# Kernel tuning notes

Hardware: AMD Instinct MI355X
Metric: run time of the kernel (lower is better)

## Reference

```python
import jax, jax.numpy as jnp
import numpy as np

B, N, C = 4, 1024, 256
E = 65536
HID = 256  # LAYERS = [256, 256, 256]

def _linear_init(key, out_dim, in_dim):
    kw, kb = jax.random.split(key)
    s = 1.0 / np.sqrt(in_dim)
    W = jax.random.uniform(kw, (out_dim, in_dim), jnp.float32, -s, s)
    b = jax.random.uniform(kb, (out_dim,), jnp.float32, -s, s)
    return W, b

def setup_inputs() -> dict:
    key = jax.random.key(0)
    ks = jax.random.split(key, 5)
    pooled_features = jax.random.normal(ks[0], (B, N, C), jnp.float32)
    edge_index = jax.random.randint(ks[1], (2, E), 0, B * N)  # [src; dst]
    W1, b1 = _linear_init(ks[2], HID, 2 * C)
    W2, b2 = _linear_init(ks[3], HID, 2 * HID)
    W3, b3 = _linear_init(ks[4], HID, 2 * HID)
    return {"pooled_features": pooled_features, "edge_index": edge_index,
            "W1": W1, "b1": b1, "W2": W2, "b2": b2, "W3": W3, "b3": b3}

def _edge_conv(x, src, dst, num_nodes, W, b):
    # PyG EdgeConv: x_j = x[src], x_i = x[dst]; msg = relu(fc([x_j - x_i, x_i]));
    # aggr='max' scatters messages onto dst nodes.
    x_i = x[dst]                                   # [E, d]
    x_j = x[src]                                   # [E, d]
    msg = jnp.concatenate([x_j - x_i, x_i], axis=-1)  # [E, 2d]
    msg = jax.nn.relu(msg @ W.T + b)               # [E, out]
    out = jax.ops.segment_max(msg, dst, num_segments=num_nodes)
    # empty segments -> -inf; PyG fills with 0, and relu messages are >= 0
    return jnp.maximum(out, 0.0)

def reference(pooled_features, edge_index, W1, b1, W2, b2, W3, b3):
    b_, n_, c_ = pooled_features.shape
    num_nodes = b_ * n_
    x = pooled_features.reshape(num_nodes, c_)
    src, dst = edge_index[0], edge_index[1]
    feats = [x]
    for W, bb in ((W1, b1), (W2, b2), (W3, b3)):
        x = _edge_conv(x, src, dst, num_nodes, W, bb)
        feats.append(x)
    related_features = jnp.concatenate(feats, axis=-1)  # [num_nodes, 1024]
    return related_features
```

## Files before the change

### kernel.cpp

```cpp
#include <hip/hip_runtime.h>


#define NODES 4096
#define EDGES 65536
#define OSTR 1024
#define DEGCAP 64

typedef __attribute__((ext_vector_type(8))) short bf16x8;
typedef __attribute__((ext_vector_type(4))) float f32x4;

__device__ __forceinline__ unsigned short f2bf(float f) {
    unsigned int x = __float_as_uint(f);
    return (unsigned short)((x + 0x7fff + ((x >> 16) & 1)) >> 16);
}
__device__ __forceinline__ float bf2f(unsigned short u) {
    return __uint_as_float(((unsigned int)u) << 16);
}

__device__ __forceinline__ void gemm_phase(int l, const short* Alds,
                                           const short* __restrict__ Wp,
                                           const float* __restrict__ bias,
                                           unsigned short* __restrict__ UWu,
                                           float* __restrict__ UWw,
                                           int b, int t) {
    const int wv = t >> 6, lane = t & 63;
    const int lm = lane & 15, kq = lane >> 4;
    const int nhalf = wv >> 3, sub = wv & 7;
    f32x4 acc0 = (f32x4){0.f, 0.f, 0.f, 0.f};
    f32x4 acc1 = (f32x4){0.f, 0.f, 0.f, 0.f};
    const short* ap = Alds + lm * 264 + kq * 8;
    const short* bp = Wp + (size_t)l * 131072
                         + (size_t)(nhalf * 256 + sub * 32 + lm) * 256 + kq * 8;
#pragma unroll
    for (int ks = 0; ks < 8; ++ks) {
        const int ko = ks * 32;
        bf16x8 a  = *(const bf16x8*)(ap + ko);
        bf16x8 q0 = *(const bf16x8*)(bp + ko);
        bf16x8 q1 = *(const bf16x8*)(bp + 16 * 256 + ko);
        acc0 = __builtin_amdgcn_mfma_f32_16x16x32_bf16(a, q0, acc0, 0, 0, 0);
        acc1 = __builtin_amdgcn_mfma_f32_16x16x32_bf16(a, q1, acc1, 0, 0, 0);
    }
    unsigned short* UW = UWu + (size_t)(l & 1) * NODES * 256;
#pragma unroll
    for (int nt2 = 0; nt2 < 2; ++nt2) {
        int nc = sub * 32 + nt2 * 16 + lm;
        f32x4 av = nt2 ? acc1 : acc0;
        if (nhalf == 0) {
#pragma unroll
            for (int p = 0; p < 4; ++p)
                UW[(size_t)(b * 16 + kq * 4 + p) * 256 + nc] = f2bf(av[p]);
        } else {
            float bc = bias[nc];
#pragma unroll
            for (int p = 0; p < 4; ++p)
                UWw[(size_t)(b * 16 + kq * 4 + p) * 256 + nc] = av[p] + bc;
        }
    }
}

__device__ __forceinline__ void edge_phase(int l,
                                           const unsigned short* __restrict__ UWu,
                                           const float* __restrict__ UWw,
                                           const int* __restrict__ cursor,
                                           const int* __restrict__ srcS,
                                           float* __restrict__ out,
                                           short* AldsW, int b, int t) {
    const int wv = t >> 6, lane = t & 63;
    const int i = b * 16 + wv;
    int deg = cursor[i]; if (deg > DEGCAP) deg = DEGCAP;
    const int beg = i * DEGCAP, end = beg + deg;
    const unsigned short* UW = UWu + (size_t)(l & 1) * NODES * 256;
    const float NEG = -3.4e38f;
    float mx0 = NEG, mx1 = NEG, mx2 = NEG, mx3 = NEG;
    int e = beg;
    for (; e + 8 <= end; e += 8) {
        int s0 = srcS[e + 0], s1 = srcS[e + 1], s2 = srcS[e + 2], s3 = srcS[e + 3];
        int s4 = srcS[e + 4], s5 = srcS[e + 5], s6 = srcS[e + 6], s7 = srcS[e + 7];
        ushort4 v0 = *(const ushort4*)(UW + (size_t)s0 * 256 + lane * 4);
        ushort4 v1 = *(const ushort4*)(UW + (size_t)s1 * 256 + lane * 4);
        ushort4 v2 = *(const ushort4*)(UW + (size_t)s2 * 256 + lane * 4);
        ushort4 v3 = *(const ushort4*)(UW + (size_t)s3 * 256 + lane * 4);
        ushort4 v4 = *(const ushort4*)(UW + (size_t)s4 * 256 + lane * 4);
        ushort4 v5 = *(const ushort4*)(UW + (size_t)s5 * 256 + lane * 4);
        ushort4 v6 = *(const ushort4*)(UW + (size_t)s6 * 256 + lane * 4);
        ushort4 v7 = *(const ushort4*)(UW + (size_t)s7 * 256 + lane * 4);
        mx0 = fmaxf(mx0, fmaxf(fmaxf(bf2f(v0.x), bf2f(v1.x)), fmaxf(bf2f(v2.x), bf2f(v3.x))));
        mx0 = fmaxf(mx0, fmaxf(fmaxf(bf2f(v4.x), bf2f(v5.x)), fmaxf(bf2f(v6.x), bf2f(v7.x))));
        mx1 = fmaxf(mx1, fmaxf(fmaxf(bf2f(v0.y), bf2f(v1.y)), fmaxf(bf2f(v2.y), bf2f(v3.y))));
        mx1 = fmaxf(mx1, fmaxf(fmaxf(bf2f(v4.y), bf2f(v5.y)), fmaxf(bf2f(v6.y), bf2f(v7.y))));
        mx2 = fmaxf(mx2, fmaxf(fmaxf(bf2f(v0.z), bf2f(v1.z)), fmaxf(bf2f(v2.z), bf2f(v3.z))));
        mx2 = fmaxf(mx2, fmaxf(fmaxf(bf2f(v4.z), bf2f(v5.z)), fmaxf(bf2f(v6.z), bf2f(v7.z))));
        mx3 = fmaxf(mx3, fmaxf(fmaxf(bf2f(v0.w), bf2f(v1.w)), fmaxf(bf2f(v2.w), bf2f(v3.w))));
        mx3 = fmaxf(mx3, fmaxf(fmaxf(bf2f(v4.w), bf2f(v5.w)), fmaxf(bf2f(v6.w), bf2f(v7.w))));
    }
    for (; e + 4 <= end; e += 4) {
        int s0 = srcS[e + 0], s1 = srcS[e + 1], s2 = srcS[e + 2], s3 = srcS[e + 3];
        ushort4 v0 = *(const ushort4*)(UW + (size_t)s0 * 256 + lane * 4);
        ushort4 v1 = *(const ushort4*)(UW + (size_t)s1 * 256 + lane * 4);
        ushort4 v2 = *(const ushort4*)(UW + (size_t)s2 * 256 + lane * 4);
        ushort4 v3 = *(const ushort4*)(UW + (size_t)s3 * 256 + lane * 4);
        mx0 = fmaxf(mx0, fmaxf(fmaxf(bf2f(v0.x), bf2f(v1.x)), fmaxf(bf2f(v2.x), bf2f(v3.x))));
        mx1 = fmaxf(mx1, fmaxf(fmaxf(bf2f(v0.y), bf2f(v1.y)), fmaxf(bf2f(v2.y), bf2f(v3.y))));
        mx2 = fmaxf(mx2, fmaxf(fmaxf(bf2f(v0.z), bf2f(v1.z)), fmaxf(bf2f(v2.z), bf2f(v3.z))));
        mx3 = fmaxf(mx3, fmaxf(fmaxf(bf2f(v0.w), bf2f(v1.w)), fmaxf(bf2f(v2.w), bf2f(v3.w))));
    }
    for (; e < end; ++e) {
        int s = srcS[e];
        ushort4 v = *(const ushort4*)(UW + (size_t)s * 256 + lane * 4);
        mx0 = fmaxf(mx0, bf2f(v.x)); mx1 = fmaxf(mx1, bf2f(v.y));
        mx2 = fmaxf(mx2, bf2f(v.z)); mx3 = fmaxf(mx3, bf2f(v.w));
    }
    float4 w4 = *(const float4*)(UWw + (size_t)i * 256 + lane * 4);
    f32x4 r;
    r[0] = fmaxf(mx0 + w4.x, 0.0f);
    r[1] = fmaxf(mx1 + w4.y, 0.0f);
    r[2] = fmaxf(mx2 + w4.z, 0.0f);
    r[3] = fmaxf(mx3 + w4.w, 0.0f);
    *(f32x4*)(out + (size_t)i * OSTR + (l + 1) * 256 + lane * 4) = r;
    if (AldsW) {
        ushort4 rb;
        rb.x = f2bf(r[0]); rb.y = f2bf(r[1]); rb.z = f2bf(r[2]); rb.w = f2bf(r[3]);
        *(ushort4*)(AldsW + wv * 264 + lane * 4) = rb;
    }
}

__global__ __launch_bounds__(256) void k_prep(const float* __restrict__ x0,
                                              const int* __restrict__ srcIdx,
                                              const int* __restrict__ dstIdx,
                                              const float* __restrict__ W0,
                                              const float* __restrict__ W1,
                                              const float* __restrict__ W2,
                                              float* __restrict__ out,
                                              short* __restrict__ Wp,
                                              int* __restrict__ cursor,
                                              int* __restrict__ srcS) {
    int tid = blockIdx.x * 256 + threadIdx.x;
    f32x4 v = ((const f32x4*)x0)[tid];
    ((f32x4*)out)[(size_t)(tid >> 6) * 256 + (tid & 63)] = v;
    for (int q = tid; q < 393216; q += 262144) {
        int layer = q >> 17, idx = q & 131071;
        const float* W = layer == 0 ? W0 : (layer == 1 ? W1 : W2);
        int n2 = idx >> 8, c = idx & 255;
        float wv2 = (n2 < 256) ? W[n2 * 512 + c]
                               : W[(n2 - 256) * 512 + 256 + c] - W[(n2 - 256) * 512 + c];
        Wp[q] = (short)f2bf(wv2);
    }
    if (tid < EDGES) {
        int d = dstIdx[tid];
        int p = atomicAdd(&cursor[d], 1);
        if (p < DEGCAP) srcS[d * DEGCAP + p] = srcIdx[tid];
    }
}

__global__ __launch_bounds__(1024, 4) void k_g0(const float* __restrict__ x0,
                                                const short* __restrict__ Wp,
                                                const float* __restrict__ B0,
                                                unsigned short* __restrict__ UWu,
                                                float* __restrict__ UWw) {
    __shared__ __align__(16) short Alds[16 * 264];
    const int t = threadIdx.x, b = blockIdx.x;
    {
        int row = t >> 6, c4 = t & 63;
        f32x4 v = *((const f32x4*)x0 + (size_t)(b * 16 + row) * 64 + c4);
        ushort4 hb;
        hb.x = f2bf(v[0]); hb.y = f2bf(v[1]); hb.z = f2bf(v[2]); hb.w = f2bf(v[3]);
        *(ushort4*)(Alds + row * 264 + c4 * 4) = hb;
    }
    __syncthreads();
    gemm_phase(0, Alds, Wp, B0, UWu, UWw, b, t);
}

__global__ __launch_bounds__(1024, 4) void k_eg(int l,
                                                const short* __restrict__ Wp,
                                                const float* __restrict__ biasN,
                                                unsigned short* __restrict__ UWu,
                                                float* __restrict__ UWw,
                                                const int* __restrict__ cursor,
                                                const int* __restrict__ srcS,
                                                float* __restrict__ out) {
    __shared__ __align__(16) short Alds[16 * 264];
    const int t = threadIdx.x, b = blockIdx.x;
    edge_phase(l, UWu, UWw, cursor, srcS, out, Alds, b, t);
    __syncthreads();
    gemm_phase(l + 1, Alds, Wp, biasN, UWu, UWw, b, t);
}

__global__ __launch_bounds__(1024, 4) void k_e2(const unsigned short* __restrict__ UWu,
                                                const float* __restrict__ UWw,
                                                const int* __restrict__ cursor,
                                                const int* __restrict__ srcS,
                                                float* __restrict__ out) {
    const int t = threadIdx.x, b = blockIdx.x;
    edge_phase(2, UWu, UWw, cursor, srcS, out, (short*)nullptr, b, t);
}

extern "C" void kernel_launch(void* const* d_in, const int* in_sizes, int n_in,
                              void* d_out, int out_size, void* d_ws, size_t ws_size,
                              hipStream_t stream) {
    const float* x0 = (const float*)d_in[0];
    const int* ei = (const int*)d_in[1];
    const int* srcIdx = ei;
    const int* dstIdx = ei + EDGES;
    float* out = (float*)d_out;

    char* w = (char*)d_ws;
    unsigned short* UWu = (unsigned short*)w;
    float* UWw = (float*)(w + 4194304);
    short* Wp = (short*)(w + 8388608);
    int* srcS = (int*)(w + 9175040);
    int* cursor = (int*)(w + 10223616);

    (void)hipMemsetAsync((void*)cursor, 0, 16384, stream);

    const float* W0 = (const float*)d_in[2]; const float* B0 = (const float*)d_in[3];
    const float* W1 = (const float*)d_in[4]; const float* B1 = (const float*)d_in[5];
    const float* W2 = (const float*)d_in[6]; const float* B2 = (const float*)d_in[7];

    k_prep<<<1024, 256, 0, stream>>>(x0, srcIdx, dstIdx, W0, W1, W2, out, Wp, cursor, srcS);
    k_g0<<<256, 1024, 0, stream>>>(x0, Wp, B0, UWu, UWw);
    k_eg<<<256, 1024, 0, stream>>>(0, Wp, B1, UWu, UWw, cursor, srcS, out);
    k_eg<<<256, 1024, 0, stream>>>(1, Wp, B2, UWu, UWw, cursor, srcS, out);
    k_e2<<<256, 1024, 0, stream>>>(UWu, UWw, cursor, srcS, out);
}
```

Measured before the change: 132.1 us.

## Fuse prep into first GEMM kernel and preload weight fragments into registers

Merges the prep kernel (input copy, CSR build, weight packing) with the layer-0 GEMM into one launch. Layer-0 weights are read straight from fp32 W0 and converted to bf16 in registers, so only layers 1-2 are packed into Wp, which shrinks the workspace. In the edge+GEMM kernels, each wave loads its weight fragments into registers before the edge phase so that the load latency overlaps the gather. The cost is more register pressure under 1024-thread blocks, and each layer-0 block redundantly re-reads and converts W0 from fp32.

After: 150.6 us. 1.14x slower.

```diff
diff --git a/kernel.cpp b/kernel.cpp
--- a/kernel.cpp
+++ b/kernel.cpp
@@ -16,31 +16,34 @@
 __device__ __forceinline__ float bf2f(unsigned short u) {
     return __uint_as_float(((unsigned int)u) << 16);
 }
-
-__device__ __forceinline__ void gemm_phase(int l, const short* Alds,
-                                           const short* __restrict__ Wp,
-                                           const float* __restrict__ bias,
-                                           unsigned short* __restrict__ UWu,
-                                           float* __restrict__ UWw,
-                                           int b, int t) {
+__device__ __forceinline__ bf16x8 pack8(float4 a, float4 b) {
+    bf16x8 r;
+    r[0] = (short)f2bf(a.x); r[1] = (short)f2bf(a.y);
+    r[2] = (short)f2bf(a.z); r[3] = (short)f2bf(a.w);
+    r[4] = (short)f2bf(b.x); r[5] = (short)f2bf(b.y);
+    r[6] = (short)f2bf(b.z); r[7] = (short)f2bf(b.w);
+    return r;
+}
+
+__device__ __forceinline__ void gemm_regs(int par, const bf16x8 fb[2][8],
+                                          const short* Alds,
+                                          const float* __restrict__ bias,
+                                          unsigned short* __restrict__ UWu,
+                                          float* __restrict__ UWw,
+                                          int b, int t) {
     const int wv = t >> 6, lane = t & 63;
     const int lm = lane & 15, kq = lane >> 4;
     const int nhalf = wv >> 3, sub = wv & 7;
     f32x4 acc0 = (f32x4){0.f, 0.f, 0.f, 0.f};
     f32x4 acc1 = (f32x4){0.f, 0.f, 0.f, 0.f};
     const short* ap = Alds + lm * 264 + kq * 8;
-    const short* bp = Wp + (size_t)l * 131072
-                         + (size_t)(nhalf * 256 + sub * 32 + lm) * 256 + kq * 8;
 #pragma unroll
     for (int ks = 0; ks < 8; ++ks) {
-        const int ko = ks * 32;
-        bf16x8 a  = *(const bf16x8*)(ap + ko);
-        bf16x8 q0 = *(const bf16x8*)(bp + ko);
-        bf16x8 q1 = *(const bf16x8*)(bp + 16 * 256 + ko);
-        acc0 = __builtin_amdgcn_mfma_f32_16x16x32_bf16(a, q0, acc0, 0, 0, 0);
-        acc1 = __builtin_amdgcn_mfma_f32_16x16x32_bf16(a, q1, acc1, 0, 0, 0);
-    }
-    unsigned short* UW = UWu + (size_t)(l & 1) * NODES * 256;
+        bf16x8 a = *(const bf16x8*)(ap + ks * 32);
+        acc0 = __builtin_amdgcn_mfma_f32_16x16x32_bf16(a, fb[0][ks], acc0, 0, 0, 0);
+        acc1 = __builtin_amdgcn_mfma_f32_16x16x32_bf16(a, fb[1][ks], acc1, 0, 0, 0);
+    }
+    unsigned short* UW = UWu + (size_t)par * NODES * 256;
 #pragma unroll
     for (int nt2 = 0; nt2 < 2; ++nt2) {
         int nc = sub * 32 + nt2 * 16 + lm;
@@ -124,50 +127,74 @@
     }
 }
 
-__global__ __launch_bounds__(256) void k_prep(const float* __restrict__ x0,
-                                              const int* __restrict__ srcIdx,
-                                              const int* __restrict__ dstIdx,
-                                              const float* __restrict__ W0,
-                                              const float* __restrict__ W1,
-                                              const float* __restrict__ W2,
-                                              float* __restrict__ out,
-                                              short* __restrict__ Wp,
-                                              int* __restrict__ cursor,
-                                              int* __restrict__ srcS) {
-    int tid = blockIdx.x * 256 + threadIdx.x;
-    f32x4 v = ((const f32x4*)x0)[tid];
-    ((f32x4*)out)[(size_t)(tid >> 6) * 256 + (tid & 63)] = v;
-    for (int q = tid; q < 393216; q += 262144) {
-        int layer = q >> 17, idx = q & 131071;
-        const float* W = layer == 0 ? W0 : (layer == 1 ? W1 : W2);
+__global__ __launch_bounds__(1024, 4) void k_p0(const float* __restrict__ x0,
+                                                const int* __restrict__ srcIdx,
+                                                const int* __restrict__ dstIdx,
+                                                const float* __restrict__ W0,
+                                                const float* __restrict__ W1,
+                                                const float* __restrict__ W2,
+                                                const float* __restrict__ B0,
+                                                float* __restrict__ out,
+                                                short* __restrict__ Wp,
+                                                unsigned short* __restrict__ UWu,
+                                                float* __restrict__ UWw,
+                                                int* __restrict__ cursor,
+                                                int* __restrict__ srcS) {
+    __shared__ __align__(16) short Alds[16 * 264];
+    const int t = threadIdx.x, b = blockIdx.x;
+    const int gtid = b * 1024 + t;
+    {
+        f32x4 v = ((const f32x4*)x0)[gtid];
+        ((f32x4*)out)[(size_t)(gtid >> 6) * 256 + (gtid & 63)] = v;
+        ushort4 hb;
+        hb.x = f2bf(v[0]); hb.y = f2bf(v[1]); hb.z = f2bf(v[2]); hb.w = f2bf(v[3]);
+        *(ushort4*)(Alds + (t >> 6) * 264 + (t & 63) * 4) = hb;
+
+        int layer = gtid >> 17, idx = gtid & 131071;
+        const float* W = layer == 0 ? W1 : W2;
         int n2 = idx >> 8, c = idx & 255;
         float wv2 = (n2 < 256) ? W[n2 * 512 + c]
                                : W[(n2 - 256) * 512 + 256 + c] - W[(n2 - 256) * 512 + c];
-        Wp[q] = (short)f2bf(wv2);
-    }
-    if (tid < EDGES) {
-        int d = dstIdx[tid];
-        int p = atomicAdd(&cursor[d], 1);
-        if (p < DEGCAP) srcS[d * DEGCAP + p] = srcIdx[tid];
-    }
-}
-
-__global__ __launch_bounds__(1024, 4) void k_g0(const float* __restrict__ x0,
-                                                const short* __restrict__ Wp,
-                                                const float* __restrict__ B0,
-                                                unsigned short* __restrict__ UWu,
-                                                float* __restrict__ UWw) {
-    __shared__ __align__(16) short Alds[16 * 264];
-    const int t = threadIdx.x, b = blockIdx.x;
+        Wp[gtid] = (short)f2bf(wv2);
+
+        if (gtid < EDGES) {
+            int d = dstIdx[gtid];
+            int p = atomicAdd(&cursor[d], 1);
+            if (p < DEGCAP) srcS[d * DEGCAP + p] = srcIdx[gtid];
+        }
+    }
+    __syncthreads();
+    const int wv = t >> 6, lane = t & 63;
+    const int lm = lane & 15, kq = lane >> 4;
+    const int nhalf = wv >> 3, sub = wv & 7;
+    bf16x8 fb[2][8];
     {
-        int row = t >> 6, c4 = t & 63;
-        f32x4 v = *((const f32x4*)x0 + (size_t)(b * 16 + row) * 64 + c4);
-        ushort4 hb;
-        hb.x = f2bf(v[0]); hb.y = f2bf(v[1]); hb.z = f2bf(v[2]); hb.w = f2bf(v[3]);
-        *(ushort4*)(Alds + row * 264 + c4 * 4) = hb;
-    }
-    __syncthreads();
-    gemm_phase(0, Alds, Wp, B0, UWu, UWw, b, t);
+        const int r0 = sub * 32 + lm;
+#pragma unroll
+        for (int rr = 0; rr < 2; ++rr) {
+            const float* rp = W0 + (size_t)(r0 + rr * 16) * 512 + kq * 8;
+#pragma unroll
+            for (int ks = 0; ks < 8; ++ks) {
+                const int ko = ks * 32;
+                if (nhalf == 0) {
+                    fb[rr][ks] = pack8(*(const float4*)(rp + ko),
+                                       *(const float4*)(rp + ko + 4));
+                } else {
+                    float4 a0 = *(const float4*)(rp + ko);
+                    float4 a1 = *(const float4*)(rp + ko + 4);
+                    float4 c0 = *(const float4*)(rp + 256 + ko);
+                    float4 c1 = *(const float4*)(rp + 256 + ko + 4);
+                    float4 d0, d1;
+                    d0.x = c0.x - a0.x; d0.y = c0.y - a0.y;
+                    d0.z = c0.z - a0.z; d0.w = c0.w - a0.w;
+                    d1.x = c1.x - a1.x; d1.y = c1.y - a1.y;
+                    d1.z = c1.z - a1.z; d1.w = c1.w - a1.w;
+                    fb[rr][ks] = pack8(d0, d1);
+                }
+            }
+        }
+    }
+    gemm_regs(0, fb, Alds, B0, UWu, UWw, b, t);
 }
 
 __global__ __launch_bounds__(1024, 4) void k_eg(int l,
@@ -180,9 +207,22 @@
                                                 float* __restrict__ out) {
     __shared__ __align__(16) short Alds[16 * 264];
     const int t = threadIdx.x, b = blockIdx.x;
+    const int lane = t & 63;
+    const int lm = lane & 15, kq = lane >> 4;
+    const int wv = t >> 6, nhalf = wv >> 3, sub = wv & 7;
+    bf16x8 fb[2][8];
+    {
+        const short* bp = Wp + (size_t)l * 131072
+                             + (size_t)(nhalf * 256 + sub * 32 + lm) * 256 + kq * 8;
+#pragma unroll
+        for (int ks = 0; ks < 8; ++ks) {
+            fb[0][ks] = *(const bf16x8*)(bp + ks * 32);
+            fb[1][ks] = *(const bf16x8*)(bp + 16 * 256 + ks * 32);
+        }
+    }
     edge_phase(l, UWu, UWw, cursor, srcS, out, Alds, b, t);
     __syncthreads();
-    gemm_phase(l + 1, Alds, Wp, biasN, UWu, UWw, b, t);
+    gemm_regs((l + 1) & 1, fb, Alds, biasN, UWu, UWw, b, t);
 }
 
 __global__ __launch_bounds__(1024, 4) void k_e2(const unsigned short* __restrict__ UWu,
@@ -207,8 +247,8 @@
     unsigned short* UWu = (unsigned short*)w;
     float* UWw = (float*)(w + 4194304);
     short* Wp = (short*)(w + 8388608);
-    int* srcS = (int*)(w + 9175040);
-    int* cursor = (int*)(w + 10223616);
+    int* srcS = (int*)(w + 8912896);
+    int* cursor = (int*)(w + 9961472);
 
     (void)hipMemsetAsync((void*)cursor, 0, 16384, stream);
 
@@ -216,8 +256,8 @@
     const float* W1 = (const float*)d_in[4]; const float* B1 = (const float*)d_in[5];
     const float* W2 = (const float*)d_in[6]; const float* B2 = (const float*)d_in[7];
 
-    k_prep<<<1024, 256, 0, stream>>>(x0, srcIdx, dstIdx, W0, W1, W2, out, Wp, cursor, srcS);
-    k_g0<<<256, 1024, 0, stream>>>(x0, Wp, B0, UWu, UWw);
+    k_p0<<<256, 1024, 0, stream>>>(x0, srcIdx, dstIdx, W0, W1, W2, B0,
+                                   out, Wp, UWu, UWw, cursor, srcS);
     k_eg<<<256, 1024, 0, stream>>>(0, Wp, B1, UWu, UWw, cursor, srcS, out);
     k_eg<<<256, 1024, 0, stream>>>(1, Wp, B2, UWu, UWw, cursor, srcS, out);
     k_e2<<<256, 1024, 0, stream>>>(UWu, UWw, cursor, srcS, out);
```
